# Optimization experiments

Measured on AMD Instinct MI355X. Metric: run time of the kernel, lower is better.

Reference implementation:

```python
import jax, jax.numpy as jnp
import numpy as np

HEAD_DIM = 64
N_HEADS = 32
N_KV = 8
ROPE_BASE = 500000.0
FREQ_CONFIG = {"factor": 32.0, "low_freq_factor": 1.0, "high_freq_factor": 4.0, "original_context_length": 8192}


def _rope_tables(head_dim, theta, n_pos, fc):
    # faithful to precompute_rope_params with llama3 freq scaling
    inv_freq = 1.0 / theta ** (np.arange(0, head_dim, 2, dtype=np.float32) / head_dim)
    low_wl = fc["original_context_length"] / fc["low_freq_factor"]
    high_wl = fc["original_context_length"] / fc["high_freq_factor"]
    wavelen = 2.0 * np.pi / inv_freq
    inv_l = np.where(wavelen > low_wl, inv_freq / fc["factor"], inv_freq)
    smooth = (fc["original_context_length"] / wavelen - fc["low_freq_factor"]) / (fc["high_freq_factor"] - fc["low_freq_factor"])
    smoothed = (1.0 - smooth) * (inv_freq / fc["factor"]) + smooth * inv_freq
    med = (wavelen <= low_wl) & (wavelen >= high_wl)
    inv_freq = np.where(med, smoothed, inv_l)
    pos = np.arange(n_pos, dtype=np.float32)
    angles = pos[:, None] * inv_freq[None, :]          # [T, head_dim/2]
    angles = np.concatenate([angles, angles], axis=1)  # [T, head_dim]
    return jnp.asarray(np.cos(angles), jnp.float32), jnp.asarray(np.sin(angles), jnp.float32)


def _apply_rope(x, cos, sin):
    # x: [b, h, t, d]; cos/sin: [t, d]
    d = x.shape[-1]
    x1, x2 = x[..., : d // 2], x[..., d // 2:]
    rotated = jnp.concatenate([-x2, x1], axis=-1)
    return x * cos[None, None] + rotated * sin[None, None]


def setup_inputs() -> dict:
    key = jax.random.key(0)
    ks = jax.random.split(key, 5)
    b, t, d = 1, 2048, 2048
    s = 0.02
    return {
        "x": jax.random.normal(ks[0], (b, t, d), jnp.float32),
        "Wq": jax.random.normal(ks[1], (d, d), jnp.float32) * s,
        "Wk": jax.random.normal(ks[2], (N_KV * HEAD_DIM, d), jnp.float32) * s,
        "Wv": jax.random.normal(ks[3], (N_KV * HEAD_DIM, d), jnp.float32) * s,
        "Wo": jax.random.normal(ks[4], (d, d), jnp.float32) * s,
        "start_pos": 0,
    }


def reference(x, Wq, Wk, Wv, Wo, start_pos):
    b, t, _ = x.shape
    cos, sin = _rope_tables(HEAD_DIM, ROPE_BASE, start_pos + t, FREQ_CONFIG)
    cos, sin = cos[start_pos:start_pos + t], sin[start_pos:start_pos + t]

    q = (x @ Wq.T).reshape(b, t, N_HEADS, HEAD_DIM).transpose(0, 2, 1, 3)  # [b,H,t,d]
    k = (x @ Wk.T).reshape(b, t, N_KV, HEAD_DIM).transpose(0, 2, 1, 3)     # [b,G,t,d]
    v = (x @ Wv.T).reshape(b, t, N_KV, HEAD_DIM).transpose(0, 2, 1, 3)

    q = _apply_rope(q, cos, sin)
    k = _apply_rope(k, cos, sin)

    n_rep = N_HEADS // N_KV
    k = jnp.repeat(k, n_rep, axis=1)  # [b,H,t,d]
    v = jnp.repeat(v, n_rep, axis=1)

    scores = jnp.einsum("bhqd,bhkd->bhqk", q, k)
    causal = jnp.triu(jnp.ones((t, t), bool), k=1)
    scores = jnp.where(causal[None, None], -jnp.inf, scores) / jnp.sqrt(jnp.float32(HEAD_DIM))
    weights = jax.nn.softmax(scores, axis=-1)
    ctx = jnp.einsum("bhqk,bhkd->bhqd", weights, v)
    ctx = ctx.transpose(0, 2, 1, 3).reshape(b, t, N_HEADS * HEAD_DIM)
    return ctx @ Wo.T
```

## Files before the change

kernel.cpp:

```cpp
#include <hip/hip_runtime.h>
#include <math.h>

#define T_SEQ 2048
#define D_MODEL 2048
#define HEAD_DIM 64
#define N_HEADS 32
#define N_KV 8

using short8 = __attribute__((ext_vector_type(8))) short;
using f32x4  = __attribute__((ext_vector_type(4))) float;
using f32x16 = __attribute__((ext_vector_type(16))) float;
using u32x4  = __attribute__((ext_vector_type(4))) unsigned int;

#define MFMA16(a, b, c) __builtin_amdgcn_mfma_f32_16x16x32_bf16(a, b, c, 0, 0, 0)
#define MFMA32(a, b, c) __builtin_amdgcn_mfma_f32_32x32x16_bf16(a, b, c, 0, 0, 0)

__device__ __forceinline__ unsigned short f2bf(float f) {
    unsigned int u = __builtin_bit_cast(unsigned int, f);
    u += 0x7fff + ((u >> 16) & 1);
    return (unsigned short)(u >> 16);
}
__device__ __forceinline__ void gld_lds16(const ushort* g, ushort* l) {
    __builtin_amdgcn_global_load_lds((const __attribute__((address_space(1))) void*)g,
                                     (__attribute__((address_space(3))) void*)l, 16, 0, 0);
}
__device__ __forceinline__ unsigned int cvtpk(float lo, float hi) {
    unsigned int r;
    asm("v_cvt_pk_bf16_f32 %0, %1, %2" : "=v"(r) : "v"(lo), "v"(hi));
    return r;
}
__device__ __forceinline__ void plswap(unsigned int& a, unsigned int& b) {
    auto r = __builtin_amdgcn_permlane32_swap(a, b, false, false);
    a = r[0];
    b = r[1];
}

__global__ __launch_bounds__(256) void rope_tables_kernel(float* __restrict__ cosT, float* __restrict__ sinT,
                                                          const int* __restrict__ start_pos, int T) {
    int idx = blockIdx.x * 256 + threadIdx.x;
    int t = idx >> 5;
    int i = idx & 31;
    float pos = (float)(start_pos[0] + t);
    float expo = (float)i / 32.0f;
    float inv_freq = 1.0f / powf(500000.0f, expo);
    const float two_pi = 6.283185307179586f;
    float wavelen = two_pi / inv_freq;
    const float low_wl = 8192.0f;
    const float high_wl = 2048.0f;
    float inv;
    if (wavelen > low_wl) {
        inv = inv_freq / 32.0f;
    } else if (wavelen < high_wl) {
        inv = inv_freq;
    } else {
        float smooth = (8192.0f / wavelen - 1.0f) / 3.0f;
        inv = (1.0f - smooth) * (inv_freq / 32.0f) + smooth * inv_freq;
    }
    float ang = pos * inv;
    cosT[i * T + t] = cosf(ang);
    sinT[i * T + t] = sinf(ang);
}

__global__ __launch_bounds__(256) void cast_all_kernel(
    const float* __restrict__ x, const float* __restrict__ wq,
    const float* __restrict__ wk, const float* __restrict__ wv,
    const float* __restrict__ wo,
    ushort* __restrict__ xb, ushort* __restrict__ wqb,
    ushort* __restrict__ wkb, ushort* __restrict__ wvb, ushort* __restrict__ wob) {
    int i = blockIdx.x * 256 + threadIdx.x;
    const float* src; ushort* dst; int off;
    if (i < 1048576)      { src = x;  dst = xb;  off = i; }
    else if (i < 2097152) { src = wq; dst = wqb; off = i - 1048576; }
    else if (i < 2359296) { src = wk; dst = wkb; off = i - 2097152; }
    else if (i < 2621440) { src = wv; dst = wvb; off = i - 2359296; }
    else                  { src = wo; dst = wob; off = i - 2621440; }
    float4 v = ((const float4*)src)[off];
    ushort4 o;
    o.x = f2bf(v.x); o.y = f2bf(v.y); o.z = f2bf(v.z); o.w = f2bf(v.w);
    ((ushort4*)dst)[off] = o;
}

__global__ __launch_bounds__(256) void gemm_qkv(
    const ushort* __restrict__ X, const ushort* __restrict__ Wqb,
    const ushort* __restrict__ Wkb, const ushort* __restrict__ Wvb,
    ushort* __restrict__ Qo, ushort* __restrict__ Ko, ushort* __restrict__ Vto,
    const float* __restrict__ cosT, const float* __restrict__ sinT,
    int T, int D) {
    __shared__ __align__(16) ushort As[2][2][2048];
    __shared__ __align__(16) ushort Bs[2][2][4096];
    const int tid = threadIdx.x;
    const int w = tid >> 6, l = tid & 63;
    const int m0 = blockIdx.x * 64;
    const int n0g = blockIdx.y * 128;

    const ushort* B;
    ushort* Cout;
    int n0, doRope;
    if (n0g < 2048)      { B = Wqb + (size_t)n0g * D;          Cout = Qo;  n0 = n0g;        doRope = 1; }
    else if (n0g < 2560) { B = Wkb + (size_t)(n0g - 2048) * D; Cout = Ko;  n0 = n0g - 2048; doRope = 1; }
    else                 { B = Wvb + (size_t)(n0g - 2560) * D; Cout = Vto; n0 = n0g - 2560; doRope = 0; }

    const int wm = (w >> 1) * 32, wn = (w & 1) * 64;
    const int lr = l & 15;
    const int quad = l >> 4;

    f32x4 zero = {0.f, 0.f, 0.f, 0.f};
    f32x4 acc[2][4];
#pragma unroll
    for (int i = 0; i < 2; ++i)
#pragma unroll
        for (int j = 0; j < 4; ++j) acc[i][j] = zero;

    const int srow = l >> 2;
    const int scg  = ((l & 3) ^ (srow & 3)) * 8;
    const ushort* Ag  = X + (size_t)(m0 + 16 * w + srow) * D + scg;
    const ushort* Bg0 = B + (size_t)(16 * (2 * w) + srow) * D + scg;
    const ushort* Bg1 = B + (size_t)(16 * (2 * w + 1) + srow) * D + scg;

#define GSTAGE(k0v, nb) { \
    gld_lds16(Ag  + (k0v),      &As[nb][0][w * 512]); \
    gld_lds16(Ag  + (k0v) + 32, &As[nb][1][w * 512]); \
    gld_lds16(Bg0 + (k0v),      &Bs[nb][0][(2 * w) * 512]); \
    gld_lds16(Bg0 + (k0v) + 32, &Bs[nb][1][(2 * w) * 512]); \
    gld_lds16(Bg1 + (k0v),      &Bs[nb][0][(2 * w + 1) * 512]); \
    gld_lds16(Bg1 + (k0v) + 32, &Bs[nb][1][(2 * w + 1) * 512]); }

    GSTAGE(0, 0);

    const int rsw = (quad ^ (lr & 3)) * 8;
    for (int k0 = 0; k0 < D; k0 += 64) {
        const int b = (k0 >> 6) & 1;
        __syncthreads();
        if (k0 + 64 < D) GSTAGE(k0 + 64, b ^ 1);
#pragma unroll
        for (int sub = 0; sub < 2; ++sub) {
            short8 af[2], bf[4];
#pragma unroll
            for (int i = 0; i < 2; ++i) af[i] = *(const short8*)&As[b][sub][(wm + i * 16 + lr) * 32 + rsw];
#pragma unroll
            for (int j = 0; j < 4; ++j) bf[j] = *(const short8*)&Bs[b][sub][(wn + j * 16 + lr) * 32 + rsw];
#pragma unroll
            for (int i = 0; i < 2; ++i)
#pragma unroll
                for (int j = 0; j < 4; ++j)
                    acc[i][j] = MFMA16(af[i], bf[j], acc[i][j]);
        }
    }
#undef GSTAGE

    const int mbase = m0 + wm + quad * 4;
    if (doRope) {
        const float qsc = (n0g < 2048) ? 0.18033688011112042f : 1.0f;
#pragma unroll
        for (int i = 0; i < 2; ++i) {
            int trow = mbase + i * 16;
#pragma unroll
            for (int j = 0; j < 2; ++j) {
                int i1 = lr + j * 16;
                float4 c4 = *(const float4*)&cosT[(size_t)i1 * T + trow];
                float4 s4 = *(const float4*)&sinT[(size_t)i1 * T + trow];
                int n1 = n0 + wn + lr + j * 16;
                int n2 = n1 + 32;
                size_t b1 = (size_t)(n1 >> 6) * ((size_t)T * 64) + (size_t)(n1 & 63);
                size_t b2 = (size_t)(n2 >> 6) * ((size_t)T * 64) + (size_t)(n2 & 63);
                float cs[4] = {c4.x, c4.y, c4.z, c4.w};
                float sn[4] = {s4.x, s4.y, s4.z, s4.w};
#pragma unroll
                for (int r = 0; r < 4; ++r) {
                    float x1 = acc[i][j][r], x2 = acc[i][j + 2][r];
                    Cout[b1 + (size_t)(trow + r) * 64] = f2bf((x1 * cs[r] - x2 * sn[r]) * qsc);
                    Cout[b2 + (size_t)(trow + r) * 64] = f2bf((x2 * cs[r] + x1 * sn[r]) * qsc);
                }
            }
        }
    } else {
#pragma unroll
        for (int i = 0; i < 2; ++i)
#pragma unroll
            for (int j = 0; j < 4; ++j) {
                int n = n0 + wn + lr + j * 16;
                int m = mbase + i * 16;
                ushort4 o;
                o.x = f2bf(acc[i][j][0]); o.y = f2bf(acc[i][j][1]);
                o.z = f2bf(acc[i][j][2]); o.w = f2bf(acc[i][j][3]);
                *(ushort4*)&Vto[(size_t)n * T + m] = o;
            }
    }
}

__global__ __launch_bounds__(256) void gemm_bt_f32(const ushort* __restrict__ A,
                                                   const ushort* __restrict__ B,
                                                   float* __restrict__ C,
                                                   int M, int N, int K) {
    __shared__ __align__(16) ushort As[2][2][2048];
    __shared__ __align__(16) ushort Bs[2][2][4096];
    const int tid = threadIdx.x;
    const int w = tid >> 6, l = tid & 63;
    const int m0 = blockIdx.x * 64, n0 = blockIdx.y * 128;
    const int wm = (w >> 1) * 32, wn = (w & 1) * 64;
    const int lr = l & 15;
    const int quad = l >> 4;

    f32x4 zero = {0.f, 0.f, 0.f, 0.f};
    f32x4 acc[2][4];
#pragma unroll
    for (int i = 0; i < 2; ++i)
#pragma unroll
        for (int j = 0; j < 4; ++j) acc[i][j] = zero;

    const int srow = l >> 2;
    const int scg  = ((l & 3) ^ (srow & 3)) * 8;
    const ushort* Ag  = A + (size_t)(m0 + 16 * w + srow) * K + scg;
    const ushort* Bg0 = B + (size_t)(n0 + 16 * (2 * w) + srow) * K + scg;
    const ushort* Bg1 = B + (size_t)(n0 + 16 * (2 * w + 1) + srow) * K + scg;

#define GSTAGE(k0v, nb) { \
    gld_lds16(Ag  + (k0v),      &As[nb][0][w * 512]); \
    gld_lds16(Ag  + (k0v) + 32, &As[nb][1][w * 512]); \
    gld_lds16(Bg0 + (k0v),      &Bs[nb][0][(2 * w) * 512]); \
    gld_lds16(Bg0 + (k0v) + 32, &Bs[nb][1][(2 * w) * 512]); \
    gld_lds16(Bg1 + (k0v),      &Bs[nb][0][(2 * w + 1) * 512]); \
    gld_lds16(Bg1 + (k0v) + 32, &Bs[nb][1][(2 * w + 1) * 512]); }

    GSTAGE(0, 0);

    const int rsw = (quad ^ (lr & 3)) * 8;
    for (int k0 = 0; k0 < K; k0 += 64) {
        const int b = (k0 >> 6) & 1;
        __syncthreads();
        if (k0 + 64 < K) GSTAGE(k0 + 64, b ^ 1);
#pragma unroll
        for (int sub = 0; sub < 2; ++sub) {
            short8 af[2], bf[4];
#pragma unroll
            for (int i = 0; i < 2; ++i) af[i] = *(const short8*)&As[b][sub][(wm + i * 16 + lr) * 32 + rsw];
#pragma unroll
            for (int j = 0; j < 4; ++j) bf[j] = *(const short8*)&Bs[b][sub][(wn + j * 16 + lr) * 32 + rsw];
#pragma unroll
            for (int i = 0; i < 2; ++i)
#pragma unroll
                for (int j = 0; j < 4; ++j)
                    acc[i][j] = MFMA16(af[i], bf[j], acc[i][j]);
        }
    }
#undef GSTAGE

    const int mbase = m0 + wm + quad * 4;
    const int nbase = n0 + wn + lr;
#pragma unroll
    for (int i = 0; i < 2; ++i)
#pragma unroll
        for (int j = 0; j < 4; ++j)
#pragma unroll
            for (int r = 0; r < 4; ++r)
                C[(size_t)(mbase + i * 16 + r) * N + (nbase + j * 16)] = acc[i][j][r];
}

__global__ __launch_bounds__(256, 2) void attn_mfma(const ushort* __restrict__ Q,
                                                    const ushort* __restrict__ K,
                                                    const ushort* __restrict__ Vt,
                                                    ushort* __restrict__ ctx, int T) {
    __shared__ __align__(16) ushort Ks[3][4096];
    __shared__ __align__(16) ushort Vs[3][4096];
    const int tid = threadIdx.x, w = tid >> 6, l = tid & 63;
    const int lq = l & 31, hi = l >> 5;
    const int hp = blockIdx.y;
    const int hk = hp >> 1;
    const int h  = 2 * hp + (w & 1);
    const int roff = (w >> 1) * 32;
    const int bx = blockIdx.x;
    const int qt = ((hp >> 3) & 1) ? (31 - bx) : bx;
    const int ntiles = qt + 1;
    const int qbase = qt * 64;
    const int qrow = qbase + roff + lq;
    const ushort* Kb = K + (size_t)hk * T * 64;
    const ushort* Vb = Vt + (size_t)hk * 64 * T;

    const int srow = l >> 3;
    const int sc   = ((l & 7) ^ srow) * 8;

    const ushort* Qrow = Q + ((size_t)h * T + qrow) * 64;
    short8 qf[4];
#pragma unroll
    for (int ks = 0; ks < 4; ++ks)
        qf[ks] = *(const short8*)(Qrow + ks * 16 + hi * 8);

    f32x16 oacc0, oacc1;
#pragma unroll
    for (int r = 0; r < 16; ++r) { oacc0[r] = 0.f; oacc1[r] = 0.f; }
    float ls[4] = {0.f, 0.f, 0.f, 0.f};

#define ASTAGE(kt, buf) do { \
    size_t _k0 = (size_t)(kt) * 64; \
    const int _c0 = 2 * w, _c1 = 2 * w + 1; \
    gld_lds16(Kb + (_k0 + _c0 * 8 + srow) * 64 + sc, &Ks[buf][_c0 * 512]); \
    gld_lds16(Kb + (_k0 + _c1 * 8 + srow) * 64 + sc, &Ks[buf][_c1 * 512]); \
    gld_lds16(Vb + (size_t)(_c0 * 8 + srow) * T + _k0 + sc, &Vs[buf][_c0 * 512]); \
    gld_lds16(Vb + (size_t)(_c1 * 8 + srow) * T + _k0 + sc, &Vs[buf][_c1 * 512]); \
} while (0)

#define QKT(bn, sd0, sd1, skip1) do { \
    __builtin_amdgcn_s_setprio(1); \
    _Pragma("unroll") \
    for (int ks = 0; ks < 4; ++ks) { \
        const int c = ((ks * 2 + hi) ^ (lq & 7)) * 8; \
        short8 kf0 = *(const short8*)&Ks[bn][lq * 64 + c]; \
        sd0 = MFMA32(kf0, qf[ks], sd0); \
    } \
    if (!(skip1)) { \
        _Pragma("unroll") \
        for (int ks = 0; ks < 4; ++ks) { \
            const int c = ((ks * 2 + hi) ^ (lq & 7)) * 8; \
            short8 kf1 = *(const short8*)&Ks[bn][(lq + 32) * 64 + c]; \
            sd1 = MFMA32(kf1, qf[ks], sd1); \
        } \
    } \
    __builtin_amdgcn_s_setprio(0); \
} while (0)

    ASTAGE(0, 0);
    if (ntiles > 1) {
        ASTAGE(1, 1);
        asm volatile("s_waitcnt vmcnt(6)" ::: "memory");
    } else {
        asm volatile("s_waitcnt vmcnt(2)" ::: "memory");
    }
    __builtin_amdgcn_s_barrier();
    __builtin_amdgcn_sched_barrier(0);

    f32x16 s_cur0, s_cur1, s_next0, s_next1;
#pragma unroll
    for (int r = 0; r < 16; ++r) { s_cur0[r] = 0.f; s_cur1[r] = 0.f; }
    QKT(0, s_cur0, s_cur1, (ntiles == 1) && (roff == 0));

    int b = 0;
    for (int kt = 0; kt < ntiles; ++kt) {
        if (kt + 1 < ntiles) asm volatile("s_waitcnt vmcnt(2)" ::: "memory");
        else                 asm volatile("s_waitcnt vmcnt(0)" ::: "memory");
        __builtin_amdgcn_s_barrier();
        __builtin_amdgcn_sched_barrier(0);

        const int k0 = kt * 64;
        const bool last  = (kt == ntiles - 1);
        const bool halfT = last && (roff == 0);

        if (kt + 1 < ntiles) {
            int bn = b + 1; if (bn == 3) bn = 0;
            const bool halfN = (kt + 1 == ntiles - 1) && (roff == 0);
#pragma unroll
            for (int r = 0; r < 16; ++r) { s_next0[r] = 0.f; s_next1[r] = 0.f; }
            QKT(bn, s_next0, s_next1, halfN);
        }
        if (kt + 2 < ntiles) {
            int bs = b + 2; if (bs >= 3) bs -= 3;
            ASTAGE(kt + 2, bs);
        }

        f32x16 p0, p1;
        if (last) {
            if (roff == 0) {
#pragma unroll
                for (int r = 0; r < 16; ++r) {
                    const int kk = k0 + (r & 3) + 8 * (r >> 2) + 4 * hi;
                    p0[r] = (kk <= qrow) ? __builtin_amdgcn_exp2f(s_cur0[r]) : 0.f;
                }
            } else {
#pragma unroll
                for (int r = 0; r < 16; ++r) p0[r] = __builtin_amdgcn_exp2f(s_cur0[r]);
#pragma unroll
                for (int r = 0; r < 16; ++r) {
                    const int kk = k0 + 32 + (r & 3) + 8 * (r >> 2) + 4 * hi;
                    p1[r] = (kk <= qrow) ? __builtin_amdgcn_exp2f(s_cur1[r]) : 0.f;
                }
            }
        } else {
#pragma unroll
            for (int r = 0; r < 16; ++r) p0[r] = __builtin_amdgcn_exp2f(s_cur0[r]);
#pragma unroll
            for (int r = 0; r < 16; ++r) p1[r] = __builtin_amdgcn_exp2f(s_cur1[r]);
        }
#pragma unroll
        for (int r = 0; r < 16; ++r) ls[r & 3] += p0[r];
        if (!halfT) {
#pragma unroll
            for (int r = 0; r < 16; ++r) ls[r & 3] += p1[r];
        }

        const int nks2 = halfT ? 2 : 4;
        __builtin_amdgcn_s_setprio(1);
        for (int ks2 = 0; ks2 < nks2; ++ks2) {
            const f32x16& pp = (ks2 < 2) ? p0 : p1;
            const int bse = (ks2 & 1) * 8;
            unsigned int a0 = cvtpk(pp[bse + 0], pp[bse + 1]);
            unsigned int a1 = cvtpk(pp[bse + 2], pp[bse + 3]);
            unsigned int b0 = cvtpk(pp[bse + 4], pp[bse + 5]);
            unsigned int b1 = cvtpk(pp[bse + 6], pp[bse + 7]);
            plswap(a0, b0);
            plswap(a1, b1);
            u32x4 tw = {a0, a1, b0, b1};
            short8 pf = __builtin_bit_cast(short8, tw);
            const int c = ((ks2 * 2 + hi) ^ (lq & 7)) * 8;
            short8 vf0 = *(const short8*)&Vs[b][lq * 64 + c];
            short8 vf1 = *(const short8*)&Vs[b][(lq + 32) * 64 + c];
            oacc0 = MFMA32(vf0, pf, oacc0);
            oacc1 = MFMA32(vf1, pf, oacc1);
        }
        __builtin_amdgcn_s_setprio(0);

        s_cur0 = s_next0;
        s_cur1 = s_next1;
        if (++b == 3) b = 0;
    }
#undef QKT
#undef ASTAGE

    float vsum = (ls[0] + ls[1]) + (ls[2] + ls[3]);
    vsum += __shfl_xor(vsum, 32, 64);
    const float inv = 1.f / vsum;

    ushort* cp = ctx + (size_t)qrow * 2048 + h * 64;
#pragma unroll
    for (int g = 0; g < 4; ++g) {
        ushort4 o0, o1;
        o0.x = f2bf(oacc0[4 * g + 0] * inv); o0.y = f2bf(oacc0[4 * g + 1] * inv);
        o0.z = f2bf(oacc0[4 * g + 2] * inv); o0.w = f2bf(oacc0[4 * g + 3] * inv);
        *(ushort4*)&cp[g * 8 + hi * 4] = o0;
        o1.x = f2bf(oacc1[4 * g + 0] * inv); o1.y = f2bf(oacc1[4 * g + 1] * inv);
        o1.z = f2bf(oacc1[4 * g + 2] * inv); o1.w = f2bf(oacc1[4 * g + 3] * inv);
        *(ushort4*)&cp[32 + g * 8 + hi * 4] = o1;
    }
}

extern "C" void kernel_launch(void* const* d_in, const int* in_sizes, int n_in,
                              void* d_out, int out_size, void* d_ws, size_t ws_size,
                              hipStream_t stream) {
    const float* x  = (const float*)d_in[0];
    const float* Wq = (const float*)d_in[1];
    const float* Wk = (const float*)d_in[2];
    const float* Wv = (const float*)d_in[3];
    const float* Wo = (const float*)d_in[4];
    const int* start_pos = (const int*)d_in[5];
    float* out = (float*)d_out;

    const int T = T_SEQ, D = D_MODEL;
    const int KV = N_KV * HEAD_DIM;

    char* w = (char*)d_ws;
    float* cosT = (float*)w;            w += (size_t)32 * T * 4;
    float* sinT = (float*)w;            w += (size_t)32 * T * 4;
    ushort* xbf  = (ushort*)w;          w += (size_t)T * D * 2;
    ushort* wqbf = (ushort*)w;          w += (size_t)D * D * 2;
    ushort* wkbf = (ushort*)w;          w += (size_t)KV * D * 2;
    ushort* wvbf = (ushort*)w;          w += (size_t)KV * D * 2;
    ushort* wobf = (ushort*)w;          w += (size_t)D * D * 2;
    ushort* qbf  = (ushort*)w;          w += (size_t)N_HEADS * T * 64 * 2;
    ushort* kbf  = (ushort*)w;          w += (size_t)N_KV * T * 64 * 2;
    ushort* vtbf = (ushort*)w;          w += (size_t)N_KV * 64 * T * 2;
    ushort* ctxbf = xbf;

    rope_tables_kernel<<<dim3((T * 32) / 256), dim3(256), 0, stream>>>(cosT, sinT, start_pos, T);

    cast_all_kernel<<<dim3(14336), dim3(256), 0, stream>>>(x, Wq, Wk, Wv, Wo,
                                                           xbf, wqbf, wkbf, wvbf, wobf);

    gemm_qkv<<<dim3(T / 64, (D + 2 * KV) / 128), dim3(256), 0, stream>>>(
        xbf, wqbf, wkbf, wvbf, qbf, kbf, vtbf, cosT, sinT, T, D);

    attn_mfma<<<dim3(32, 16), dim3(256), 0, stream>>>(qbf, kbf, vtbf, ctxbf, T);

    gemm_bt_f32<<<dim3(T / 64, D / 128), dim3(256), 0, stream>>>(ctxbf, wobf, out, T, D, D);
}
```

Baseline: 206.1 us.

## Split attention KV range across blocks with atomic fp32 accumulation and normalize pass

```diff
diff --git a/kernel.cpp b/kernel.cpp
--- a/kernel.cpp
+++ b/kernel.cpp
@@ -35,38 +35,37 @@
     b = r[1];
 }
 
-__global__ __launch_bounds__(256) void rope_tables_kernel(float* __restrict__ cosT, float* __restrict__ sinT,
-                                                          const int* __restrict__ start_pos, int T) {
-    int idx = blockIdx.x * 256 + threadIdx.x;
-    int t = idx >> 5;
-    int i = idx & 31;
-    float pos = (float)(start_pos[0] + t);
-    float expo = (float)i / 32.0f;
-    float inv_freq = 1.0f / powf(500000.0f, expo);
-    const float two_pi = 6.283185307179586f;
-    float wavelen = two_pi / inv_freq;
-    const float low_wl = 8192.0f;
-    const float high_wl = 2048.0f;
-    float inv;
-    if (wavelen > low_wl) {
-        inv = inv_freq / 32.0f;
-    } else if (wavelen < high_wl) {
-        inv = inv_freq;
-    } else {
-        float smooth = (8192.0f / wavelen - 1.0f) / 3.0f;
-        inv = (1.0f - smooth) * (inv_freq / 32.0f) + smooth * inv_freq;
-    }
-    float ang = pos * inv;
-    cosT[i * T + t] = cosf(ang);
-    sinT[i * T + t] = sinf(ang);
-}
-
-__global__ __launch_bounds__(256) void cast_all_kernel(
+__global__ __launch_bounds__(256) void cast_rope_kernel(
     const float* __restrict__ x, const float* __restrict__ wq,
     const float* __restrict__ wk, const float* __restrict__ wv,
     const float* __restrict__ wo,
     ushort* __restrict__ xb, ushort* __restrict__ wqb,
-    ushort* __restrict__ wkb, ushort* __restrict__ wvb, ushort* __restrict__ wob) {
+    ushort* __restrict__ wkb, ushort* __restrict__ wvb, ushort* __restrict__ wob,
+    float* __restrict__ cosT, float* __restrict__ sinT,
+    const int* __restrict__ start_pos, int T) {
+    if (blockIdx.x >= 14336) {
+        int idx = (blockIdx.x - 14336) * 256 + threadIdx.x;
+        int t = idx >> 5;
+        int i = idx & 31;
+        float pos = (float)(start_pos[0] + t);
+        float expo = (float)i / 32.0f;
+        float inv_freq = 1.0f / powf(500000.0f, expo);
+        const float two_pi = 6.283185307179586f;
+        float wavelen = two_pi / inv_freq;
+        float inv;
+        if (wavelen > 8192.0f) {
+            inv = inv_freq / 32.0f;
+        } else if (wavelen < 2048.0f) {
+            inv = inv_freq;
+        } else {
+            float smooth = (8192.0f / wavelen - 1.0f) / 3.0f;
+            inv = (1.0f - smooth) * (inv_freq / 32.0f) + smooth * inv_freq;
+        }
+        float ang = pos * inv;
+        cosT[i * T + t] = cosf(ang);
+        sinT[i * T + t] = sinf(ang);
+        return;
+    }
     int i = blockIdx.x * 256 + threadIdx.x;
     const float* src; ushort* dst; int off;
     if (i < 1048576)      { src = x;  dst = xb;  off = i; }
@@ -256,23 +255,29 @@
                 C[(size_t)(mbase + i * 16 + r) * N + (nbase + j * 16)] = acc[i][j][r];
 }
 
-__global__ __launch_bounds__(256, 2) void attn_mfma(const ushort* __restrict__ Q,
+__global__ __launch_bounds__(256, 3) void attn_mfma(const ushort* __restrict__ Q,
                                                     const ushort* __restrict__ K,
                                                     const ushort* __restrict__ Vt,
-                                                    ushort* __restrict__ ctx, int T) {
-    __shared__ __align__(16) ushort Ks[3][4096];
-    __shared__ __align__(16) ushort Vs[3][4096];
+                                                    float* __restrict__ ctxT,
+                                                    float* __restrict__ lacc, int T) {
+    __shared__ __align__(16) ushort Ks[2][4096];
+    __shared__ __align__(16) ushort Vs[2][4096];
     const int tid = threadIdx.x, w = tid >> 6, l = tid & 63;
     const int lq = l & 31, hi = l >> 5;
-    const int hp = blockIdx.y;
+
+    const int bid = blockIdx.x;
+    int hp, qt, c;
+    if (bid < 512)       { int i = bid;        qt = 31 - (i >> 6); hp = (i >> 2) & 15; c = i & 3; }
+    else if (bid < 896)  { int i = bid - 512;  qt = 23 - i / 48;   hp = (i / 3) & 15;  c = i % 3; }
+    else if (bid < 1152) { int i = bid - 896;  qt = 15 - (i >> 5); hp = (i >> 1) & 15; c = i & 1; }
+    else                 { int i = bid - 1152; qt = 7 - (i >> 4);  hp = i & 15;        c = 0; }
+    const int t0 = 8 * c;
+    const int t1 = (8 * c + 8 < qt + 1) ? (8 * c + 8) : (qt + 1);
+
     const int hk = hp >> 1;
     const int h  = 2 * hp + (w & 1);
     const int roff = (w >> 1) * 32;
-    const int bx = blockIdx.x;
-    const int qt = ((hp >> 3) & 1) ? (31 - bx) : bx;
-    const int ntiles = qt + 1;
-    const int qbase = qt * 64;
-    const int qrow = qbase + roff + lq;
+    const int qrow = qt * 64 + roff + lq;
     const ushort* Kb = K + (size_t)hk * T * 64;
     const ushort* Vb = Vt + (size_t)hk * 64 * T;
 
@@ -290,106 +295,101 @@
     for (int r = 0; r < 16; ++r) { oacc0[r] = 0.f; oacc1[r] = 0.f; }
     float ls[4] = {0.f, 0.f, 0.f, 0.f};
 
-#define ASTAGE(kt, buf) do { \
+#define KSTAGE(kt, buf) do { \
     size_t _k0 = (size_t)(kt) * 64; \
-    const int _c0 = 2 * w, _c1 = 2 * w + 1; \
-    gld_lds16(Kb + (_k0 + _c0 * 8 + srow) * 64 + sc, &Ks[buf][_c0 * 512]); \
-    gld_lds16(Kb + (_k0 + _c1 * 8 + srow) * 64 + sc, &Ks[buf][_c1 * 512]); \
-    gld_lds16(Vb + (size_t)(_c0 * 8 + srow) * T + _k0 + sc, &Vs[buf][_c0 * 512]); \
-    gld_lds16(Vb + (size_t)(_c1 * 8 + srow) * T + _k0 + sc, &Vs[buf][_c1 * 512]); \
+    gld_lds16(Kb + (_k0 + (2 * w) * 8 + srow) * 64 + sc,     &Ks[buf][(2 * w) * 512]); \
+    gld_lds16(Kb + (_k0 + (2 * w + 1) * 8 + srow) * 64 + sc, &Ks[buf][(2 * w + 1) * 512]); \
+} while (0)
+#define VSTAGE(kt, buf) do { \
+    size_t _k0 = (size_t)(kt) * 64; \
+    gld_lds16(Vb + (size_t)((2 * w) * 8 + srow) * T + _k0 + sc,     &Vs[buf][(2 * w) * 512]); \
+    gld_lds16(Vb + (size_t)((2 * w + 1) * 8 + srow) * T + _k0 + sc, &Vs[buf][(2 * w + 1) * 512]); \
 } while (0)
 
 #define QKT(bn, sd0, sd1, skip1) do { \
     __builtin_amdgcn_s_setprio(1); \
     _Pragma("unroll") \
     for (int ks = 0; ks < 4; ++ks) { \
-        const int c = ((ks * 2 + hi) ^ (lq & 7)) * 8; \
-        short8 kf0 = *(const short8*)&Ks[bn][lq * 64 + c]; \
+        const int cc = ((ks * 2 + hi) ^ (lq & 7)) * 8; \
+        short8 kf0 = *(const short8*)&Ks[bn][lq * 64 + cc]; \
         sd0 = MFMA32(kf0, qf[ks], sd0); \
     } \
     if (!(skip1)) { \
         _Pragma("unroll") \
         for (int ks = 0; ks < 4; ++ks) { \
-            const int c = ((ks * 2 + hi) ^ (lq & 7)) * 8; \
-            short8 kf1 = *(const short8*)&Ks[bn][(lq + 32) * 64 + c]; \
+            const int cc = ((ks * 2 + hi) ^ (lq & 7)) * 8; \
+            short8 kf1 = *(const short8*)&Ks[bn][(lq + 32) * 64 + cc]; \
             sd1 = MFMA32(kf1, qf[ks], sd1); \
         } \
     } \
     __builtin_amdgcn_s_setprio(0); \
 } while (0)
 
-    ASTAGE(0, 0);
-    if (ntiles > 1) {
-        ASTAGE(1, 1);
-        asm volatile("s_waitcnt vmcnt(6)" ::: "memory");
-    } else {
-        asm volatile("s_waitcnt vmcnt(2)" ::: "memory");
-    }
+    KSTAGE(t0, 0);
+    const bool two = (t0 + 1 < t1);
+    if (two) KSTAGE(t0 + 1, 1);
+    VSTAGE(t0, 0);
+    if (two) asm volatile("s_waitcnt vmcnt(4)" ::: "memory");
+    else     asm volatile("s_waitcnt vmcnt(2)" ::: "memory");
     __builtin_amdgcn_s_barrier();
     __builtin_amdgcn_sched_barrier(0);
 
     f32x16 s_cur0, s_cur1, s_next0, s_next1;
 #pragma unroll
     for (int r = 0; r < 16; ++r) { s_cur0[r] = 0.f; s_cur1[r] = 0.f; }
-    QKT(0, s_cur0, s_cur1, (ntiles == 1) && (roff == 0));
-
-    int b = 0;
-    for (int kt = 0; kt < ntiles; ++kt) {
-        if (kt + 1 < ntiles) asm volatile("s_waitcnt vmcnt(2)" ::: "memory");
-        else                 asm volatile("s_waitcnt vmcnt(0)" ::: "memory");
+    QKT(0, s_cur0, s_cur1, (t0 == qt) && (roff == 0));
+
+    for (int kt = t0; kt < t1; ++kt) {
+        const int b = kt & 1;
+        asm volatile("s_waitcnt vmcnt(0)" ::: "memory");
         __builtin_amdgcn_s_barrier();
         __builtin_amdgcn_sched_barrier(0);
 
+        const bool lastg = (kt == qt);
+        const bool halfT = lastg && (roff == 0);
+
+        if (kt + 1 < t1) {
+#pragma unroll
+            for (int r = 0; r < 16; ++r) { s_next0[r] = 0.f; s_next1[r] = 0.f; }
+            QKT(b ^ 1, s_next0, s_next1, ((kt + 1) == qt) && (roff == 0));
+        }
+        if (kt + 2 < t1) KSTAGE(kt + 2, b);
+        if (kt + 1 < t1) VSTAGE(kt + 1, b ^ 1);
+
         const int k0 = kt * 64;
-        const bool last  = (kt == ntiles - 1);
-        const bool halfT = last && (roff == 0);
-
-        if (kt + 1 < ntiles) {
-            int bn = b + 1; if (bn == 3) bn = 0;
-            const bool halfN = (kt + 1 == ntiles - 1) && (roff == 0);
-#pragma unroll
-            for (int r = 0; r < 16; ++r) { s_next0[r] = 0.f; s_next1[r] = 0.f; }
-            QKT(bn, s_next0, s_next1, halfN);
-        }
-        if (kt + 2 < ntiles) {
-            int bs = b + 2; if (bs >= 3) bs -= 3;
-            ASTAGE(kt + 2, bs);
-        }
-
-        f32x16 p0, p1;
-        if (last) {
+        if (lastg) {
             if (roff == 0) {
 #pragma unroll
                 for (int r = 0; r < 16; ++r) {
                     const int kk = k0 + (r & 3) + 8 * (r >> 2) + 4 * hi;
-                    p0[r] = (kk <= qrow) ? __builtin_amdgcn_exp2f(s_cur0[r]) : 0.f;
+                    s_cur0[r] = (kk <= qrow) ? __builtin_amdgcn_exp2f(s_cur0[r]) : 0.f;
                 }
             } else {
 #pragma unroll
-                for (int r = 0; r < 16; ++r) p0[r] = __builtin_amdgcn_exp2f(s_cur0[r]);
+                for (int r = 0; r < 16; ++r) s_cur0[r] = __builtin_amdgcn_exp2f(s_cur0[r]);
 #pragma unroll
                 for (int r = 0; r < 16; ++r) {
                     const int kk = k0 + 32 + (r & 3) + 8 * (r >> 2) + 4 * hi;
-                    p1[r] = (kk <= qrow) ? __builtin_amdgcn_exp2f(s_cur1[r]) : 0.f;
+                    s_cur1[r] = (kk <= qrow) ? __builtin_amdgcn_exp2f(s_cur1[r]) : 0.f;
                 }
             }
         } else {
 #pragma unroll
-            for (int r = 0; r < 16; ++r) p0[r] = __builtin_amdgcn_exp2f(s_cur0[r]);
-#pragma unroll
-            for (int r = 0; r < 16; ++r) p1[r] = __builtin_amdgcn_exp2f(s_cur1[r]);
-        }
-#pragma unroll
-        for (int r = 0; r < 16; ++r) ls[r & 3] += p0[r];
+            for (int r = 0; r < 16; ++r) s_cur0[r] = __builtin_amdgcn_exp2f(s_cur0[r]);
+#pragma unroll
+            for (int r = 0; r < 16; ++r) s_cur1[r] = __builtin_amdgcn_exp2f(s_cur1[r]);
+        }
+#pragma unroll
+        for (int r = 0; r < 16; ++r) ls[r & 3] += s_cur0[r];
         if (!halfT) {
 #pragma unroll
-            for (int r = 0; r < 16; ++r) ls[r & 3] += p1[r];
+            for (int r = 0; r < 16; ++r) ls[r & 3] += s_cur1[r];
         }
 
         const int nks2 = halfT ? 2 : 4;
         __builtin_amdgcn_s_setprio(1);
         for (int ks2 = 0; ks2 < nks2; ++ks2) {
-            const f32x16& pp = (ks2 < 2) ? p0 : p1;
+            const f32x16& pp = (ks2 < 2) ? s_cur0 : s_cur1;
             const int bse = (ks2 & 1) * 8;
             unsigned int a0 = cvtpk(pp[bse + 0], pp[bse + 1]);
             unsigned int a1 = cvtpk(pp[bse + 2], pp[bse + 3]);
@@ -399,9 +399,9 @@
             plswap(a1, b1);
             u32x4 tw = {a0, a1, b0, b1};
             short8 pf = __builtin_bit_cast(short8, tw);
-            const int c = ((ks2 * 2 + hi) ^ (lq & 7)) * 8;
-            short8 vf0 = *(const short8*)&Vs[b][lq * 64 + c];
-            short8 vf1 = *(const short8*)&Vs[b][(lq + 32) * 64 + c];
+            const int cc = ((ks2 * 2 + hi) ^ (lq & 7)) * 8;
+            short8 vf0 = *(const short8*)&Vs[b][lq * 64 + cc];
+            short8 vf1 = *(const short8*)&Vs[b][(lq + 32) * 64 + cc];
             oacc0 = MFMA32(vf0, pf, oacc0);
             oacc1 = MFMA32(vf1, pf, oacc1);
         }
@@ -409,25 +409,55 @@
 
         s_cur0 = s_next0;
         s_cur1 = s_next1;
-        if (++b == 3) b = 0;
     }
 #undef QKT
-#undef ASTAGE
+#undef KSTAGE
+#undef VSTAGE
 
     float vsum = (ls[0] + ls[1]) + (ls[2] + ls[3]);
     vsum += __shfl_xor(vsum, 32, 64);
-    const float inv = 1.f / vsum;
-
-    ushort* cp = ctx + (size_t)qrow * 2048 + h * 64;
-#pragma unroll
-    for (int g = 0; g < 4; ++g) {
-        ushort4 o0, o1;
-        o0.x = f2bf(oacc0[4 * g + 0] * inv); o0.y = f2bf(oacc0[4 * g + 1] * inv);
-        o0.z = f2bf(oacc0[4 * g + 2] * inv); o0.w = f2bf(oacc0[4 * g + 3] * inv);
-        *(ushort4*)&cp[g * 8 + hi * 4] = o0;
-        o1.x = f2bf(oacc1[4 * g + 0] * inv); o1.y = f2bf(oacc1[4 * g + 1] * inv);
-        o1.z = f2bf(oacc1[4 * g + 2] * inv); o1.w = f2bf(oacc1[4 * g + 3] * inv);
-        *(ushort4*)&cp[32 + g * 8 + hi * 4] = o1;
+    if (hi == 0) atomicAdd(&lacc[(size_t)h * 2048 + qrow], vsum);
+
+    float* cb = ctxT + (size_t)(h * 64) * 2048 + qrow;
+#pragma unroll
+    for (int r = 0; r < 16; ++r) {
+        const int d = (r & 3) + 8 * (r >> 2) + 4 * hi;
+        atomicAdd(cb + (size_t)d * 2048, oacc0[r]);
+        atomicAdd(cb + (size_t)(d + 32) * 2048, oacc1[r]);
+    }
+}
+
+__global__ __launch_bounds__(256) void norm_ctx(const float* __restrict__ cT,
+                                                const float* __restrict__ lacc,
+                                                ushort* __restrict__ ctxb) {
+    __shared__ float tile[64][65];
+    const int tau = threadIdx.x;
+    const int t0 = blockIdx.x * 64;
+    const int hd0 = blockIdx.y * 64;
+    {
+        const int r = tau >> 2, cq = tau & 3;
+        const float* src = cT + (size_t)(hd0 + r) * 2048 + t0 + cq * 16;
+#pragma unroll
+        for (int j = 0; j < 4; ++j) {
+            float4 v = *(const float4*)(src + j * 4);
+            tile[r][cq * 16 + j * 4 + 0] = v.x;
+            tile[r][cq * 16 + j * 4 + 1] = v.y;
+            tile[r][cq * 16 + j * 4 + 2] = v.z;
+            tile[r][cq * 16 + j * 4 + 3] = v.w;
+        }
+    }
+    __syncthreads();
+    const int tt = tau >> 2, rq = tau & 3;
+    const float invl = 1.0f / lacc[(size_t)(hd0 >> 6) * 2048 + t0 + tt];
+    ushort* dst = ctxb + (size_t)(t0 + tt) * 2048 + hd0 + rq * 16;
+#pragma unroll
+    for (int j = 0; j < 4; ++j) {
+        ushort4 o;
+        o.x = f2bf(tile[rq * 16 + j * 4 + 0][tt] * invl);
+        o.y = f2bf(tile[rq * 16 + j * 4 + 1][tt] * invl);
+        o.z = f2bf(tile[rq * 16 + j * 4 + 2][tt] * invl);
+        o.w = f2bf(tile[rq * 16 + j * 4 + 3][tt] * invl);
+        *(ushort4*)(dst + j * 4) = o;
     }
 }
 
@@ -456,17 +486,22 @@
     ushort* qbf  = (ushort*)w;          w += (size_t)N_HEADS * T * 64 * 2;
     ushort* kbf  = (ushort*)w;          w += (size_t)N_KV * T * 64 * 2;
     ushort* vtbf = (ushort*)w;          w += (size_t)N_KV * 64 * T * 2;
-    ushort* ctxbf = xbf;
-
-    rope_tables_kernel<<<dim3((T * 32) / 256), dim3(256), 0, stream>>>(cosT, sinT, start_pos, T);
-
-    cast_all_kernel<<<dim3(14336), dim3(256), 0, stream>>>(x, Wq, Wk, Wv, Wo,
-                                                           xbf, wqbf, wkbf, wvbf, wobf);
+
+    float* ctx32T = (float*)xbf;
+    float* lacc   = (float*)wkbf;
+    ushort* ctxbf = qbf;
+
+    cast_rope_kernel<<<dim3(14336 + 256), dim3(256), 0, stream>>>(
+        x, Wq, Wk, Wv, Wo, xbf, wqbf, wkbf, wvbf, wobf, cosT, sinT, start_pos, T);
 
     gemm_qkv<<<dim3(T / 64, (D + 2 * KV) / 128), dim3(256), 0, stream>>>(
         xbf, wqbf, wkbf, wvbf, qbf, kbf, vtbf, cosT, sinT, T, D);
 
-    attn_mfma<<<dim3(32, 16), dim3(256), 0, stream>>>(qbf, kbf, vtbf, ctxbf, T);
+    hipMemsetAsync(ctx32T, 0, (size_t)2048 * 2048 * 4 + (size_t)32 * 2048 * 4, stream);
+
+    attn_mfma<<<dim3(1280), dim3(256), 0, stream>>>(qbf, kbf, vtbf, ctx32T, lacc, T);
+
+    norm_ctx<<<dim3(32, 32), dim3(256), 0, stream>>>(ctx32T, lacc, ctxbf);
 
     gemm_bt_f32<<<dim3(T / 64, D / 128), dim3(256), 0, stream>>>(ctxbf, wobf, out, T, D, D);
 }
```

Result: slower. 226.2 us (+9.7%).
